# Kernel optimization log

Hardware: AMD Instinct MI355X
Metric: run time of the kernel (lower is better)

The kernel has to match this reference:

```python
import jax, jax.numpy as jnp
import numpy as np

B, S, H, D = 4, 2048, 16, 128

def setup_inputs() -> dict:
    key = jax.random.key(0)
    kq, kk, kv = jax.random.split(key, 3)
    shape = (B, S, H, D)
    return {
        "q": jax.random.normal(kq, shape, dtype=jnp.float32),
        "k": jax.random.normal(kk, shape, dtype=jnp.float32),
        "v": jax.random.normal(kv, shape, dtype=jnp.float32),
    }

def reference(q, k, v):
    # Fused recurrent linear attention (causal, unnormalized):
    #   H_t = H_{t-1} + k_t v_t^T ;  o_t = (scale * q_t) @ H_t
    scale = jnp.asarray(q.shape[-1], q.dtype) ** -0.5
    # move seq axis to front for scan: [S, B, H, D]
    qs = jnp.moveaxis(q, 1, 0) * scale
    ks = jnp.moveaxis(k, 1, 0)
    vs = jnp.moveaxis(v, 1, 0)

    def step(h, qkv):
        qt, kt, vt = qkv  # each [B, H, D]
        h = h + kt[..., :, None] * vt[..., None, :]  # [B, H, Dk, Dv]
        o = jnp.einsum('bhk,bhkv->bhv', qt, h)       # [B, H, Dv]
        return h, o

    h0 = jnp.zeros((q.shape[0], q.shape[2], q.shape[3], v.shape[3]), dtype=q.dtype)
    _, o = jax.lax.scan(step, h0, (qs, ks, vs))
    return jnp.moveaxis(o, 0, 1)  # [B, S, H, D]
```

## Files before the change

kernel.cpp:

```cpp
#include <hip/hip_runtime.h>


#define Bc 4
#define Sq 2048
#define Hh 16
#define Dd 128
#define RS (Hh * Dd)
#define Cc 128
#define NCH (Sq / Cc)
#define BHt (Bc * Hh)
#define NSEG 2
#define CPS (NCH / NSEG)
#define SCALE 0.08838834764831845f

using frag_ab = __attribute__((ext_vector_type(8))) short;
using frag_cd = __attribute__((ext_vector_type(4))) float;

__device__ __forceinline__ unsigned short f2bf(float f) {
  union { float f; unsigned u; } x; x.f = f;
  unsigned r = x.u + 0x7FFFu + ((x.u >> 16) & 1u);
  return (unsigned short)(r >> 16);
}
__device__ __forceinline__ float bf2f(unsigned short u) {
  union { unsigned u; float f; } x; x.u = ((unsigned)u) << 16;
  return x.f;
}
__device__ __forceinline__ int sw64(int r, int c) {
  return r * 64 + ((((c >> 3) ^ (r & 7)) << 3) | (c & 7));
}
__device__ __forceinline__ int sw128(int r, int c) {
  return r * 128 + ((((c >> 3) ^ (r & 15)) << 3) | (c & 7));
}
__device__ __forceinline__ int swKT(int dk, int t) {
  return dk * 128 + ((((t >> 3) ^ (dk ^ (dk >> 4))) & 15) << 3) + (t & 7);
}
__device__ __forceinline__ int swVT(int dv, int t) {
  return dv * 128 + ((((t >> 3) ^ dv) & 15) << 3) + (t & 7);
}

__global__ __launch_bounds__(256) void phA_state(const float* __restrict__ kg,
                                                 const float* __restrict__ vg,
                                                 unsigned short* __restrict__ st) {
  __shared__ unsigned short KT[128 * 128];
  __shared__ unsigned short VT[16 * 128];
  const int tid = threadIdx.x;
  const int bh = blockIdx.x & 63;
  const int slice = (blockIdx.x >> 6) & 7;
  const int seg = blockIdx.x >> 9;
  const int b = bh >> 4, h = bh & 15;
  const int dv0 = slice * 16;
  const size_t base = (size_t)b * Sq * RS + (size_t)h * Dd;
  const int w = tid >> 6, L = tid & 63, li = L & 15, q4 = L >> 4;
  const int kdk0 = (tid & 31) * 4;
  const int ktg4 = (tid >> 5) * 4;
  const int vdv0l = (tid & 3) * 4;
  const int vt0 = (tid >> 2) * 2;

  float4 rk[4][4];
  float4 rv[2];
  auto prefetch = [&](int n) {
    const size_t t0g = (size_t)n * Cc;
#pragma unroll
    for (int p = 0; p < 4; ++p) {
      const int t0 = p * 32 + ktg4;
#pragma unroll
      for (int i = 0; i < 4; ++i)
        rk[p][i] = *(const float4*)(kg + base + (t0g + t0 + i) * (size_t)RS + kdk0);
    }
#pragma unroll
    for (int i = 0; i < 2; ++i)
      rv[i] = *(const float4*)(vg + base + (t0g + vt0 + i) * (size_t)RS + dv0 + vdv0l);
  };

  frag_cd acc[2];
  acc[0] = (frag_cd){0.f, 0.f, 0.f, 0.f};
  acc[1] = (frag_cd){0.f, 0.f, 0.f, 0.f};
  const int n0 = seg * CPS;
  prefetch(n0);
  const size_t sbb = (size_t)bh * NCH * (128 * 128);

  auto store_acc = [&](int slot) {
    const size_t sb = sbb + (size_t)slot * (128 * 128);
#pragma unroll
    for (int nt = 0; nt < 2; ++nt)
#pragma unroll
      for (int r = 0; r < 4; ++r) {
        const int dv = dv0 + 4 * q4 + r;
        const int dk = 32 * w + 16 * nt + li;
        st[sb + (size_t)dv * 128 + dk] = f2bf(acc[nt][r]);
      }
  };

  for (int j = 0; j < CPS; ++j) {
    __syncthreads();
#pragma unroll
    for (int p = 0; p < 4; ++p) {
      const int t0 = p * 32 + ktg4;
#pragma unroll
      for (int jj = 0; jj < 4; ++jj) {
        ushort4 u;
        u.x = f2bf(((const float*)&rk[p][0])[jj]);
        u.y = f2bf(((const float*)&rk[p][1])[jj]);
        u.z = f2bf(((const float*)&rk[p][2])[jj]);
        u.w = f2bf(((const float*)&rk[p][3])[jj]);
        *(ushort4*)&KT[swKT(kdk0 + jj, t0)] = u;
      }
    }
#pragma unroll
    for (int jj = 0; jj < 4; ++jj) {
      ushort2 u;
      u.x = f2bf(((const float*)&rv[0])[jj]);
      u.y = f2bf(((const float*)&rv[1])[jj]);
      *(ushort2*)&VT[swVT(vdv0l + jj, vt0)] = u;
    }
    if (j + 1 < CPS) prefetch(n0 + j + 1);
    __syncthreads();
    if (j > 0) store_acc(n0 + j);
#pragma unroll
    for (int kt = 0; kt < 4; ++kt) {
      frag_ab af = *(const frag_ab*)&VT[swVT(li, 32 * kt + 8 * q4)];
#pragma unroll
      for (int nt = 0; nt < 2; ++nt) {
        frag_ab bf = *(const frag_ab*)&KT[swKT(32 * w + 16 * nt + li, 32 * kt + 8 * q4)];
        acc[nt] = __builtin_amdgcn_mfma_f32_16x16x32_bf16(af, bf, acc[nt], 0, 0, 0);
      }
    }
  }
  if (seg + 1 < NSEG) store_acc(n0);
}

__global__ __launch_bounds__(256) void phFix(unsigned short* __restrict__ st) {
  const int bh = blockIdx.x & 63, n8 = blockIdx.x >> 6;
  const int n = 8 + n8;
  const int tid = threadIdx.x;
  const size_t b0 = ((size_t)(bh * NCH + 0)) << 14;
  const size_t bn = ((size_t)(bh * NCH + n)) << 14;
#pragma unroll
  for (int i = 0; i < 8; ++i) {
    const size_t off = (size_t)i * 2048 + tid * 8;
    const uint4 t0 = *(const uint4*)(st + b0 + off);
    if (n8 == 0) {
      *(uint4*)(st + bn + off) = t0;
    } else {
      const uint4 ln = *(const uint4*)(st + bn + off);
      const unsigned a[4] = {ln.x, ln.y, ln.z, ln.w};
      const unsigned c[4] = {t0.x, t0.y, t0.z, t0.w};
      unsigned pk[4];
#pragma unroll
      for (int e = 0; e < 4; ++e) {
        const float lo = bf2f((unsigned short)(a[e] & 0xFFFFu)) +
                         bf2f((unsigned short)(c[e] & 0xFFFFu));
        const float hi = bf2f((unsigned short)(a[e] >> 16)) +
                         bf2f((unsigned short)(c[e] >> 16));
        pk[e] = (unsigned)f2bf(lo) | ((unsigned)f2bf(hi) << 16);
      }
      uint4 out; out.x = pk[0]; out.y = pk[1]; out.z = pk[2]; out.w = pk[3];
      *(uint4*)(st + bn + off) = out;
    }
  }
}

__global__ __launch_bounds__(512) void phB_out(const float* __restrict__ qg,
                                               const float* __restrict__ kg,
                                               const float* __restrict__ vg,
                                               const unsigned short* __restrict__ st,
                                               float* __restrict__ o) {
  __shared__ unsigned short QP[128 * 128];
  __shared__ unsigned short Bb[128 * 64];
  const int tid = threadIdx.x;
  const int bid = blockIdx.x;
  const int bh = bid >> 4, n = bid & 15;
  const int b = bh >> 4, h = bh & 15;
  const size_t cbase = (size_t)b * Sq * RS + (size_t)n * Cc * RS + (size_t)h * Dd;
  const size_t sb = (size_t)(bh * 16 + n) * (128 * 128);
  const int w = tid >> 6, L = tid & 63;
  const int wr = w >> 2, wc = w & 3, li = L & 15, q4 = L >> 4;

#pragma unroll
  for (int it = 0; it < 8; ++it) {
    const int f = it * 512 + tid;
    const int t = f >> 5;
    const int c0 = (f & 31) << 2;
    const float4 q4v = *(const float4*)(qg + cbase + (size_t)t * RS + c0);
    ushort4 qu;
    qu.x = f2bf(q4v.x * SCALE); qu.y = f2bf(q4v.y * SCALE);
    qu.z = f2bf(q4v.z * SCALE); qu.w = f2bf(q4v.w * SCALE);
    *(ushort4*)&QP[sw128(t, c0)] = qu;
  }
  frag_cd accO[4][2], accP[4][2];
#pragma unroll
  for (int i = 0; i < 4; ++i)
#pragma unroll
    for (int j = 0; j < 2; ++j) {
      accO[i][j] = (frag_cd){0.f, 0.f, 0.f, 0.f};
      accP[i][j] = (frag_cd){0.f, 0.f, 0.f, 0.f};
    }

  if (n) {
    for (int half = 0; half < 2; ++half) {
      __syncthreads();
#pragma unroll
      for (int it = 0; it < 2; ++it) {
        const int f = it * 512 + tid;
        const int dv = f >> 3;
        const int c8 = (f & 7) << 3;
        const uint4 hv = *(const uint4*)(st + sb + (size_t)dv * 128 + 64 * half + c8);
        *(uint4*)&Bb[sw64(dv, c8)] = hv;
      }
      __syncthreads();
#pragma unroll
      for (int kt = 0; kt < 2; ++kt) {
        const int ktg = 2 * half + kt;
        frag_ab af[4], bf_[2];
#pragma unroll
        for (int mt = 0; mt < 4; ++mt)
          af[mt] = *(const frag_ab*)&QP[sw128(64 * wr + 16 * mt + li, 32 * ktg + 8 * q4)];
#pragma unroll
        for (int nt = 0; nt < 2; ++nt)
          bf_[nt] = *(const frag_ab*)&Bb[sw64(32 * wc + 16 * nt + li, 32 * kt + 8 * q4)];
#pragma unroll
        for (int mt = 0; mt < 4; ++mt)
#pragma unroll
          for (int nt = 0; nt < 2; ++nt)
            accO[mt][nt] = __builtin_amdgcn_mfma_f32_16x16x32_bf16(af[mt], bf_[nt], accO[mt][nt], 0, 0, 0);
      }
    }
  }

  for (int half = 0; half < 2; ++half) {
    __syncthreads();
#pragma unroll
    for (int it = 0; it < 4; ++it) {
      const int f = it * 512 + tid;
      const int t = f >> 4;
      const int c0 = (f & 15) << 2;
      const float4 k4v = *(const float4*)(kg + cbase + (size_t)t * RS + 64 * half + c0);
      ushort4 ku;
      ku.x = f2bf(k4v.x); ku.y = f2bf(k4v.y); ku.z = f2bf(k4v.z); ku.w = f2bf(k4v.w);
      *(ushort4*)&Bb[sw64(t, c0)] = ku;
    }
    __syncthreads();
    if (32 * wc <= 64 * wr + 63) {
#pragma unroll
      for (int kt = 0; kt < 2; ++kt) {
        const int ktg = 2 * half + kt;
        frag_ab af[4], bf_[2];
#pragma unroll
        for (int mt = 0; mt < 4; ++mt)
          af[mt] = *(const frag_ab*)&QP[sw128(64 * wr + 16 * mt + li, 32 * ktg + 8 * q4)];
#pragma unroll
        for (int nt = 0; nt < 2; ++nt)
          bf_[nt] = *(const frag_ab*)&Bb[sw64(32 * wc + 16 * nt + li, 32 * kt + 8 * q4)];
#pragma unroll
        for (int mt = 0; mt < 4; ++mt)
#pragma unroll
          for (int nt = 0; nt < 2; ++nt)
            if (32 * wc + 16 * nt <= 64 * wr + 16 * mt + 15)
              accP[mt][nt] = __builtin_amdgcn_mfma_f32_16x16x32_bf16(af[mt], bf_[nt], accP[mt][nt], 0, 0, 0);
      }
    }
  }
  __syncthreads();
#pragma unroll
  for (int mt = 0; mt < 4; ++mt)
#pragma unroll
    for (int nt = 0; nt < 2; ++nt) {
      const int t0 = 64 * wr + 16 * mt + 4 * q4;
      const int s = 32 * wc + 16 * nt + li;
#pragma unroll
      for (int r = 0; r < 4; ++r) {
        const int t = t0 + r;
        QP[sw128(t, s)] = (s <= t) ? f2bf(accP[mt][nt][r]) : (unsigned short)0;
      }
    }

  for (int half = 0; half < 2; ++half) {
    __syncthreads();
#pragma unroll
    for (int it = 0; it < 4; ++it) {
      const int e = (tid >> 8) | (it << 1);
      const int sl = (tid & 15) | ((e & 3) << 4);
      const int c0 = (((tid >> 4) & 15) | ((e >> 2) << 4)) << 2;
      const int s = 64 * half + sl;
      const float4 v4v = *(const float4*)(vg + cbase + (size_t)s * RS + c0);
      Bb[sw64(c0 + 0, sl)] = f2bf(v4v.x);
      Bb[sw64(c0 + 1, sl)] = f2bf(v4v.y);
      Bb[sw64(c0 + 2, sl)] = f2bf(v4v.z);
      Bb[sw64(c0 + 3, sl)] = f2bf(v4v.w);
    }
    __syncthreads();
#pragma unroll
    for (int kt = 0; kt < 2; ++kt) {
      const int ktg = 2 * half + kt;
      if (32 * ktg > 64 * wr + 63) continue;
      frag_ab af[4], bf_[2];
#pragma unroll
      for (int mt = 0; mt < 4; ++mt)
        af[mt] = *(const frag_ab*)&QP[sw128(64 * wr + 16 * mt + li, 32 * ktg + 8 * q4)];
#pragma unroll
      for (int nt = 0; nt < 2; ++nt)
        bf_[nt] = *(const frag_ab*)&Bb[sw64(32 * wc + 16 * nt + li, 32 * kt + 8 * q4)];
#pragma unroll
      for (int mt = 0; mt < 4; ++mt)
#pragma unroll
        for (int nt = 0; nt < 2; ++nt)
          if (32 * ktg <= 64 * wr + 16 * mt + 15)
            accO[mt][nt] = __builtin_amdgcn_mfma_f32_16x16x32_bf16(af[mt], bf_[nt], accO[mt][nt], 0, 0, 0);
    }
  }
#pragma unroll
  for (int mt = 0; mt < 4; ++mt)
#pragma unroll
    for (int nt = 0; nt < 2; ++nt)
#pragma unroll
      for (int r = 0; r < 4; ++r) {
        const int t = 64 * wr + 16 * mt + 4 * q4 + r;
        const int dv = 32 * wc + 16 * nt + li;
        o[cbase + (size_t)t * RS + dv] = accO[mt][nt][r];
      }
}

extern "C" void kernel_launch(void* const* d_in, const int* in_sizes, int n_in,
                              void* d_out, int out_size, void* d_ws, size_t ws_size,
                              hipStream_t stream) {
  const float* q = (const float*)d_in[0];
  const float* k = (const float*)d_in[1];
  const float* v = (const float*)d_in[2];
  float* o = (float*)d_out;
  unsigned short* st = (unsigned short*)d_ws;
  hipLaunchKernelGGL(phA_state, dim3(BHt * 8 * NSEG), dim3(256), 0, stream, k, v, st);
  hipLaunchKernelGGL(phFix, dim3(BHt * 8), dim3(256), 0, stream, st);
  hipLaunchKernelGGL(phB_out, dim3(BHt * NCH), dim3(512), 0, stream, q, k, v, st, o);
}
```

Measured before the change: 268.2 us.

## Split state scan into four segments with two-level prefix fix-up

Raises the number of sequence segments computed in parallel by the state kernel from two to four, shortening each block's serial chunk loop. The single fix-up pass is replaced by two: one that builds the carry states at segment boundaries, and one that adds each segment's carry to its three inner chunks. This trades a longer serial dependency for an extra kernel launch and more global state traffic, and adds bf16 rounding at each carry step.

```diff
diff --git a/kernel.cpp b/kernel.cpp
--- a/kernel.cpp
+++ b/kernel.cpp
@@ -9,7 +9,7 @@
 #define Cc 128
 #define NCH (Sq / Cc)
 #define BHt (Bc * Hh)
-#define NSEG 2
+#define NSEG 4
 #define CPS (NCH / NSEG)
 #define SCALE 0.08838834764831845f
 
@@ -129,34 +129,69 @@
   if (seg + 1 < NSEG) store_acc(n0);
 }
 
-__global__ __launch_bounds__(256) void phFix(unsigned short* __restrict__ st) {
-  const int bh = blockIdx.x & 63, n8 = blockIdx.x >> 6;
-  const int n = 8 + n8;
+__global__ __launch_bounds__(256) void phFixT(unsigned short* __restrict__ st) {
+  const int bh = blockIdx.x;
   const int tid = threadIdx.x;
   const size_t b0 = ((size_t)(bh * NCH + 0)) << 14;
-  const size_t bn = ((size_t)(bh * NCH + n)) << 14;
+  const size_t b4 = ((size_t)(bh * NCH + 4)) << 14;
+  const size_t b8 = ((size_t)(bh * NCH + 8)) << 14;
+  const size_t b12 = ((size_t)(bh * NCH + 12)) << 14;
 #pragma unroll
   for (int i = 0; i < 8; ++i) {
     const size_t off = (size_t)i * 2048 + tid * 8;
     const uint4 t0 = *(const uint4*)(st + b0 + off);
-    if (n8 == 0) {
-      *(uint4*)(st + bn + off) = t0;
-    } else {
-      const uint4 ln = *(const uint4*)(st + bn + off);
-      const unsigned a[4] = {ln.x, ln.y, ln.z, ln.w};
-      const unsigned c[4] = {t0.x, t0.y, t0.z, t0.w};
-      unsigned pk[4];
-#pragma unroll
-      for (int e = 0; e < 4; ++e) {
-        const float lo = bf2f((unsigned short)(a[e] & 0xFFFFu)) +
-                         bf2f((unsigned short)(c[e] & 0xFFFFu));
-        const float hi = bf2f((unsigned short)(a[e] >> 16)) +
-                         bf2f((unsigned short)(c[e] >> 16));
-        pk[e] = (unsigned)f2bf(lo) | ((unsigned)f2bf(hi) << 16);
-      }
-      uint4 out; out.x = pk[0]; out.y = pk[1]; out.z = pk[2]; out.w = pk[3];
-      *(uint4*)(st + bn + off) = out;
-    }
+    const uint4 t1 = *(const uint4*)(st + b4 + off);
+    const uint4 t2 = *(const uint4*)(st + b8 + off);
+    const unsigned a0[4] = {t0.x, t0.y, t0.z, t0.w};
+    const unsigned a1[4] = {t1.x, t1.y, t1.z, t1.w};
+    const unsigned a2[4] = {t2.x, t2.y, t2.z, t2.w};
+    unsigned p8[4], p12[4];
+#pragma unroll
+    for (int e = 0; e < 4; ++e) {
+      const float lo01 = bf2f((unsigned short)(a0[e] & 0xFFFFu)) +
+                         bf2f((unsigned short)(a1[e] & 0xFFFFu));
+      const float hi01 = bf2f((unsigned short)(a0[e] >> 16)) +
+                         bf2f((unsigned short)(a1[e] >> 16));
+      const float lo012 = lo01 + bf2f((unsigned short)(a2[e] & 0xFFFFu));
+      const float hi012 = hi01 + bf2f((unsigned short)(a2[e] >> 16));
+      p8[e] = (unsigned)f2bf(lo01) | ((unsigned)f2bf(hi01) << 16);
+      p12[e] = (unsigned)f2bf(lo012) | ((unsigned)f2bf(hi012) << 16);
+    }
+    uint4 o8, o12;
+    o8.x = p8[0]; o8.y = p8[1]; o8.z = p8[2]; o8.w = p8[3];
+    o12.x = p12[0]; o12.y = p12[1]; o12.z = p12[2]; o12.w = p12[3];
+    *(uint4*)(st + b4 + off) = t0;
+    *(uint4*)(st + b8 + off) = o8;
+    *(uint4*)(st + b12 + off) = o12;
+  }
+}
+
+__global__ __launch_bounds__(256) void phFix2(unsigned short* __restrict__ st) {
+  const int bh = blockIdx.x & 63;
+  const int idx = blockIdx.x >> 6;
+  const int s = idx / 3 + 1, j = idx % 3 + 1;
+  const int n = 4 * s + j;
+  const int tid = threadIdx.x;
+  const size_t bc = ((size_t)(bh * NCH + 4 * s)) << 14;
+  const size_t bn = ((size_t)(bh * NCH + n)) << 14;
+#pragma unroll
+  for (int i = 0; i < 8; ++i) {
+    const size_t off = (size_t)i * 2048 + tid * 8;
+    const uint4 cv = *(const uint4*)(st + bc + off);
+    const uint4 ln = *(const uint4*)(st + bn + off);
+    const unsigned a[4] = {ln.x, ln.y, ln.z, ln.w};
+    const unsigned c[4] = {cv.x, cv.y, cv.z, cv.w};
+    unsigned pk[4];
+#pragma unroll
+    for (int e = 0; e < 4; ++e) {
+      const float lo = bf2f((unsigned short)(a[e] & 0xFFFFu)) +
+                       bf2f((unsigned short)(c[e] & 0xFFFFu));
+      const float hi = bf2f((unsigned short)(a[e] >> 16)) +
+                       bf2f((unsigned short)(c[e] >> 16));
+      pk[e] = (unsigned)f2bf(lo) | ((unsigned)f2bf(hi) << 16);
+    }
+    uint4 out; out.x = pk[0]; out.y = pk[1]; out.z = pk[2]; out.w = pk[3];
+    *(uint4*)(st + bn + off) = out;
   }
 }
 
@@ -329,6 +364,7 @@
   float* o = (float*)d_out;
   unsigned short* st = (unsigned short*)d_ws;
   hipLaunchKernelGGL(phA_state, dim3(BHt * 8 * NSEG), dim3(256), 0, stream, k, v, st);
-  hipLaunchKernelGGL(phFix, dim3(BHt * 8), dim3(256), 0, stream, st);
+  hipLaunchKernelGGL(phFixT, dim3(BHt), dim3(256), 0, stream, st);
+  hipLaunchKernelGGL(phFix2, dim3(BHt * 9), dim3(256), 0, stream, st);
   hipLaunchKernelGGL(phB_out, dim3(BHt * NCH), dim3(512), 0, stream, q, k, v, st, o);
 }
```

Result: no change. 268.4 us (+0.1%).
